# Performance work log

Measured on AMD Instinct MI355X. Metric: run time of the kernel, lower is better.

## Reference

```python
import jax, jax.numpy as jnp
import numpy as np

B, C, T = 64, 22, 2560
U0, U1 = 128, 64  # lstm units per direction


def _lstm(x, Wx, Wh, b, reverse):
    """Keras-style LSTM. x:[B,T,D]. Returns (seq:[B,T,U], last:[B,U])."""
    if reverse:
        x = x[:, ::-1, :]
    U = Wh.shape[0]
    # precompute input projections for all timesteps: [T,B,4U]
    xz = (jnp.einsum('btd,dk->btk', x, Wx) + b).transpose(1, 0, 2)
    h0 = jnp.zeros((x.shape[0], U), x.dtype)
    c0 = jnp.zeros((x.shape[0], U), x.dtype)

    def step(carry, z):
        h, c = carry
        z = z + h @ Wh
        i = jax.nn.sigmoid(z[:, :U])
        f = jax.nn.sigmoid(z[:, U:2 * U])
        g = jnp.tanh(z[:, 2 * U:3 * U])
        o = jax.nn.sigmoid(z[:, 3 * U:])
        c = f * c + i * g
        h = o * jnp.tanh(c)
        return (h, c), h

    (h_last, _), hs = jax.lax.scan(step, (h0, c0), xz)
    hs = hs.transpose(1, 0, 2)  # [B,T,U]
    if reverse:
        hs = hs[:, ::-1, :]
    return hs, h_last


def setup_inputs() -> dict:
    key = jax.random.key(0)
    ks = jax.random.split(key, 20)
    s = 0.05
    d = {"x": jax.random.normal(ks[0], (B, C, T), jnp.float32)}
    # layer 0 (input dim C=22, units U0), fwd + bwd
    d["l0f_Wx"] = jax.random.normal(ks[1], (C, 4 * U0)) * s
    d["l0f_Wh"] = jax.random.normal(ks[2], (U0, 4 * U0)) * s
    d["l0f_b"] = jnp.zeros((4 * U0,))
    d["l0b_Wx"] = jax.random.normal(ks[3], (C, 4 * U0)) * s
    d["l0b_Wh"] = jax.random.normal(ks[4], (U0, 4 * U0)) * s
    d["l0b_b"] = jnp.zeros((4 * U0,))
    # layer 1 (input dim 2*U0=256, units U1), fwd + bwd
    d["l1f_Wx"] = jax.random.normal(ks[5], (2 * U0, 4 * U1)) * s
    d["l1f_Wh"] = jax.random.normal(ks[6], (U1, 4 * U1)) * s
    d["l1f_b"] = jnp.zeros((4 * U1,))
    d["l1b_Wx"] = jax.random.normal(ks[7], (2 * U0, 4 * U1)) * s
    d["l1b_Wh"] = jax.random.normal(ks[8], (U1, 4 * U1)) * s
    d["l1b_b"] = jnp.zeros((4 * U1,))
    # dense head: 2*U1=128 -> 128 -> 64 -> 1
    d["d0_W"] = jax.random.normal(ks[9], (2 * U1, 128)) * s
    d["d0_b"] = jnp.zeros((128,))
    d["d1_W"] = jax.random.normal(ks[10], (128, 64)) * s
    d["d1_b"] = jnp.zeros((64,))
    d["out_W"] = jax.random.normal(ks[11], (64, 1)) * s
    d["out_b"] = jnp.zeros((1,))
    return d


def reference(x, l0f_Wx, l0f_Wh, l0f_b, l0b_Wx, l0b_Wh, l0b_b,
              l1f_Wx, l1f_Wh, l1f_b, l1b_Wx, l1b_Wh, l1b_b,
              d0_W, d0_b, d1_W, d1_b, out_W, out_b):
    h = x.transpose(0, 2, 1)  # [B,T,C]
    # BiLSTM 0, return_sequences=True
    f_seq, _ = _lstm(h, l0f_Wx, l0f_Wh, l0f_b, reverse=False)
    b_seq, _ = _lstm(h, l0b_Wx, l0b_Wh, l0b_b, reverse=True)
    h = jnp.concatenate([f_seq, b_seq], axis=-1)  # [B,T,2*U0]
    # BiLSTM 1, return last state
    _, f_last = _lstm(h, l1f_Wx, l1f_Wh, l1f_b, reverse=False)
    _, b_last = _lstm(h, l1b_Wx, l1b_Wh, l1b_b, reverse=True)
    h = jnp.concatenate([f_last, b_last], axis=-1)  # [B,2*U1]
    # dense head (dropout inactive at inference)
    h = jax.nn.relu(h @ d0_W + d0_b)
    h = jax.nn.relu(h @ d1_W + d1_b)
    return jax.nn.sigmoid(h @ out_W + out_b)  # [B,1]
```

## Files before the change

kernel.cpp:

```cpp
#include <hip/hip_runtime.h>
#include <stdint.h>

#define TT 2560
#define BB 64
#define CC 22

typedef unsigned short ushort_t;
typedef __attribute__((ext_vector_type(4))) float floatx4;
typedef __attribute__((ext_vector_type(8))) short bf16x8;
typedef __attribute__((ext_vector_type(4))) int intx4;

__device__ __forceinline__ float bf2f(ushort_t u){
  union { uint32_t i; float f; } v; v.i = ((uint32_t)u) << 16; return v.f;
}
__device__ __forceinline__ ushort_t f2bf(float f){
  union { float f; uint32_t i; } v; v.f = f;
  uint32_t r = v.i + 0x7FFFu + ((v.i >> 16) & 1u);
  return (ushort_t)(r >> 16);
}
__device__ __forceinline__ float fsig(float x){ return 1.f/(1.f + __expf(-x)); }
__device__ __forceinline__ float ftanh(float x){ return 2.f/(1.f + __expf(-2.f*x)) - 1.f; }

__device__ __forceinline__ void ldsbar(){
  asm volatile("s_waitcnt lgkmcnt(0)\n\ts_barrier" ::: "memory");
}

__global__ __launch_bounds__(256) void k_convert_x(const float* __restrict__ x, ushort_t* __restrict__ xc){
  int i4 = blockIdx.x*256 + threadIdx.x;
  if (i4 >= BB*CC*TT/4) return;
  const float4 v = ((const float4*)x)[i4];
  uint2 o;
  o.x = (uint32_t)f2bf(v.x) | ((uint32_t)f2bf(v.y) << 16);
  o.y = (uint32_t)f2bf(v.z) | ((uint32_t)f2bf(v.w) << 16);
  ((uint2*)xc)[i4] = o;
}

__global__ __launch_bounds__(256) void k_prep_xa(const ushort_t* __restrict__ xc, ushort_t* __restrict__ xA){
  int idx = blockIdx.x*256 + threadIdx.x;
  if (idx >= BB*TT*4) return;
  int q = idx & 3;
  int rest = idx >> 2;
  int t = rest % TT, b = rest / TT;
  ushort_t v[8];
  #pragma unroll
  for (int j=0;j<8;j++){
    int c = q*8 + j;
    v[j] = (c < CC) ? xc[((size_t)b*CC + c)*TT + t] : (ushort_t)0;
  }
  *(uint4*)(xA + (size_t)idx*8) = *(const uint4*)v;
}

__global__ __launch_bounds__(256) void k_wmax(const float* __restrict__ w0f, const float* __restrict__ w0b,
                                              const float* __restrict__ w1f, const float* __restrict__ w1b,
                                              float* __restrict__ scl){
  const int b = blockIdx.x;
  const float* W = (b==0) ? w0f : (b==1) ? w0b : (b==2) ? w1f : w1b;
  const int n = (b < 2) ? 128*512 : 64*256;
  float mx = 0.f;
  for (int i = threadIdx.x; i < n; i += 256) mx = fmaxf(mx, fabsf(W[i]));
  __shared__ float red[256];
  red[threadIdx.x] = mx;
  __syncthreads();
  for (int s = 128; s > 0; s >>= 1){
    if (threadIdx.x < s) red[threadIdx.x] = fmaxf(red[threadIdx.x], red[threadIdx.x+s]);
    __syncthreads();
  }
  if (threadIdx.x == 0) scl[b] = fmaxf(red[0], 1e-8f);
}

__global__ __launch_bounds__(256) void k_prep_l0(const float* __restrict__ WxF, const float* __restrict__ WhF,
                                                 const float* __restrict__ WxB, const float* __restrict__ WhB,
                                                 const float* __restrict__ scl,
                                                 char* __restrict__ W0Q, ushort_t* __restrict__ B0X){
  int idx = blockIdx.x*256 + threadIdx.x;
  if (idx >= 2*512*160) return;
  int dir = idx / 81920; int r0 = idx % 81920; int n = r0 / 160; int k = r0 % 160;
  int g = n >> 7, u = n & 127;
  int wv = u >> 4, qq = (u >> 2) & 3, r = u & 3;
  int row = (qq*8 + wv)*16 + (r*4 + g);
  if (k < 128){
    const float* Wh = dir ? WhB : WhF;
    float sw = scl[dir];
    W0Q[(size_t)dir*65536 + row*128 + k] = (char)(int)rintf(Wh[k*512 + n] * (127.f/sw));
  } else {
    const float* Wx = dir ? WxB : WxF;
    int kx = k - 128;
    float v = (kx < CC) ? Wx[kx*512 + n] : 0.f;
    B0X[(size_t)dir*16384 + row*32 + kx] = f2bf(v);
  }
}

__global__ __launch_bounds__(256) void k_prep_l1(const float* __restrict__ WhF, const float* __restrict__ WhB,
                                                 const float* __restrict__ scl,
                                                 char* __restrict__ W1Q){
  int idx = blockIdx.x*256 + threadIdx.x;
  if (idx >= 2*256*64) return;
  int dir = idx >> 14; int r0 = idx & 16383; int n = r0 >> 6; int k = r0 & 63;
  int g = n >> 6, u = n & 63;
  int wv = u >> 4, qq = (u >> 2) & 3, r = u & 3;
  int row = (qq*4 + wv)*16 + (r*4 + g);
  const float* Wh = dir ? WhB : WhF;
  float sw = scl[2+dir];
  W1Q[(size_t)dir*16384 + row*64 + k] = (char)(int)rintf(Wh[k*256 + n] * (127.f/sw));
}

__global__ __launch_bounds__(256) void k_prep_wxT(const float* __restrict__ Wf, const float* __restrict__ Wb,
                                                  ushort_t* __restrict__ WT){
  int idx = blockIdx.x*256 + threadIdx.x;
  int dir = idx >> 16; int r = idx & 65535; int n = r >> 8; int k = r & 255;
  const float* W = dir ? Wb : Wf;
  WT[idx] = f2bf(W[k*256 + n]);
}

__global__ __launch_bounds__(512, 1) void k_lstm0m(
  const ushort_t* __restrict__ xA, const char* __restrict__ W0Q,
  const ushort_t* __restrict__ B0X, const float* __restrict__ scl,
  const float* __restrict__ bF, const float* __restrict__ bB,
  ushort_t* __restrict__ h0seq)
{
  const int dir = blockIdx.x & 1, b = blockIdx.x >> 1;
  const int tid = threadIdx.x;
  const int wv = tid >> 6, lane = tid & 63, m = lane & 15, q = lane >> 4;
  const int g  = m & 3;
  const int u  = wv*16 + q*4 + (m >> 2);
  const float* bi = dir ? bB : bF;
  const float sclc = scl[dir] * (1.f/16129.f);
  const float em = (g==2) ? -2.f : -1.f;
  const float ym = (g==2) ?  2.f :  1.f;
  const float ya = (g==2) ? -1.f :  0.f;
  const float bzl = bi[g*128 + u];

  __shared__ __align__(16) char AbufC[2][128];

  bf16x8 Bfx[4];
  intx4  BfQ[4][2];
  {
    const ushort_t* Bx = B0X + (size_t)dir*16384;
    const char*     Bq = W0Q + (size_t)dir*65536;
    #pragma unroll
    for (int qt=0; qt<4; qt++){
      int nrow = (qt*8 + wv)*16 + m;
      Bfx[qt] = *(const bf16x8*)(Bx + (size_t)nrow*32 + q*8);
      #pragma unroll
      for (int kt=0; kt<2; kt++)
        BfQ[qt][kt] = *(const intx4*)(Bq + (size_t)nrow*128 + kt*64 + q*16);
    }
  }

  if (tid < 64) ((uint32_t*)AbufC)[tid] = 0u;

  const ushort_t* xap = xA + ((size_t)b*TT*4 + q)*8;
  uint4 px[4];
  #pragma unroll
  for (int j=0; j<4; j++){
    int tj = dir ? (TT-1-j) : j;
    px[j] = *(const uint4*)(xap + (size_t)tj*32);
  }
  const ushort_t* xpp = xap + (size_t)(dir ? (TT-5) : 4)*32;
  const int xstep = dir ? -32 : 32;
  __syncthreads();

  const floatx4 z4 = {0.f,0.f,0.f,0.f};
  const intx4  zi = {0,0,0,0};
  float cst = 0.f;
  const int t00 = dir ? TT-1 : 0;
  ushort_t* hp = h0seq + ((size_t)b*TT + t00)*256 + dir*128 + u;
  const int hstep = dir ? -256 : 256;

  for (int i = 0; i < TT/4; ++i){
    #pragma unroll
    for (int p = 0; p < 4; ++p){
      const int s = i*4 + p;
      const int cur = s & 1, nxt = cur ^ 1;

      const char* ar = &AbufC[cur][0];
      intx4 AfQ0 = *(const intx4*)(ar + q*16);
      intx4 AfQ1 = *(const intx4*)(ar + 64 + q*16);
      bf16x8 Ax = *(const bf16x8*)&px[p];

      floatx4 ax0 = __builtin_amdgcn_mfma_f32_16x16x32_bf16(Ax, Bfx[0], z4, 0,0,0);
      floatx4 ax1 = __builtin_amdgcn_mfma_f32_16x16x32_bf16(Ax, Bfx[1], z4, 0,0,0);
      floatx4 ax2 = __builtin_amdgcn_mfma_f32_16x16x32_bf16(Ax, Bfx[2], z4, 0,0,0);
      floatx4 ax3 = __builtin_amdgcn_mfma_f32_16x16x32_bf16(Ax, Bfx[3], z4, 0,0,0);

      intx4 aq0 = __builtin_amdgcn_mfma_i32_16x16x64_i8(AfQ0, BfQ[0][0], zi, 0,0,0);
      intx4 aq1 = __builtin_amdgcn_mfma_i32_16x16x64_i8(AfQ0, BfQ[1][0], zi, 0,0,0);
      intx4 aq2 = __builtin_amdgcn_mfma_i32_16x16x64_i8(AfQ0, BfQ[2][0], zi, 0,0,0);
      intx4 aq3 = __builtin_amdgcn_mfma_i32_16x16x64_i8(AfQ0, BfQ[3][0], zi, 0,0,0);
      aq0 = __builtin_amdgcn_mfma_i32_16x16x64_i8(AfQ1, BfQ[0][1], aq0, 0,0,0);
      aq1 = __builtin_amdgcn_mfma_i32_16x16x64_i8(AfQ1, BfQ[1][1], aq1, 0,0,0);
      aq2 = __builtin_amdgcn_mfma_i32_16x16x64_i8(AfQ1, BfQ[2][1], aq2, 0,0,0);
      aq3 = __builtin_amdgcn_mfma_i32_16x16x64_i8(AfQ1, BfQ[3][1], aq3, 0,0,0);

      px[p] = *(const uint4*)xpp;
      xpp += xstep;

      float axs = (q < 2) ? ((q == 0) ? ax0[0] : ax1[0])
                          : ((q == 2) ? ax2[0] : ax3[0]);
      int   aqs = (q < 2) ? ((q == 0) ? aq0[0] : aq1[0])
                          : ((q == 2) ? aq2[0] : aq3[0]);

      {
        float z = (float)aqs*sclc + axs + bzl;
        float e = __expf(z * em);
        float y = 1.f/(1.f + e);
        float act = ym*y + ya;

        int ai = __float_as_int(act);
        float sf = __int_as_float(__builtin_amdgcn_ds_swizzle(ai, 0x041F));
        float sg = __int_as_float(__builtin_amdgcn_ds_swizzle(ai, 0x081F));
        float so = __int_as_float(__builtin_amdgcn_ds_swizzle(ai, 0x0C1F));

        float cc = sf*cst + act*sg;
        cst = cc;
        float hl = so*ftanh(cc);
        if (g == 0){
          AbufC[nxt][u] = (char)(int)rintf(hl * 127.f);
          *hp = f2bf(hl);
        }
        hp += hstep;
      }
      ldsbar();
    }
  }
}

__global__ __launch_bounds__(512) void k_xz1_gemm(const ushort_t* __restrict__ h0seq,
                                                  const ushort_t* __restrict__ WxT,
                                                  ushort_t* __restrict__ xz1)
{
  const int mb  = blockIdx.x;
  const int dir = blockIdx.y;
  const ushort_t* W   = WxT + (size_t)dir*256*256;
  ushort_t*       out = xz1 + (size_t)dir*BB*TT*256;
  const int wave = threadIdx.x >> 6;
  const int lane = threadIdx.x & 63;
  const int mw = wave & 3;
  const int nw = wave >> 2;
  const int m_ = lane & 15;
  const int q_ = lane >> 4;

  floatx4 acc[2][8];
  #pragma unroll
  for (int a=0;a<2;a++)
    #pragma unroll
    for (int n=0;n<8;n++) acc[a][n] = (floatx4)0.f;

  const size_t Abase = ((size_t)mb*128 + mw*32 + m_)*256 + q_*8;
  const size_t Bbase = ((size_t)nw*128 + m_)*256 + q_*8;

  for (int kc = 0; kc < 256; kc += 32){
    bf16x8 afr[2];
    #pragma unroll
    for (int mt=0;mt<2;mt++)
      afr[mt] = *(const bf16x8*)(h0seq + Abase + (size_t)mt*16*256 + kc);
    #pragma unroll
    for (int nt=0;nt<8;nt++){
      bf16x8 bfr = *(const bf16x8*)(W + Bbase + (size_t)nt*16*256 + kc);
      #pragma unroll
      for (int mt=0;mt<2;mt++)
        acc[mt][nt] = __builtin_amdgcn_mfma_f32_16x16x32_bf16(afr[mt], bfr, acc[mt][nt], 0,0,0);
    }
  }
  #pragma unroll
  for (int mt=0;mt<2;mt++)
    #pragma unroll
    for (int r=0;r<4;r++){
      size_t bt = (size_t)mb*128 + mw*32 + mt*16 + q_*4 + r;
      ushort_t* rowp = out + bt*256;
      #pragma unroll
      for (int wvz=0; wvz<4; wvz++){
        uint32_t lo = f2bf(acc[mt][wvz][r]);
        uint32_t hi = f2bf(acc[mt][wvz+4][r]);
        *(uint32_t*)(rowp + (wvz*16+m_)*4 + 2*nw) = lo | (hi << 16);
      }
    }
}

__global__ __launch_bounds__(256, 1) void k_lstm1m(
  const ushort_t* __restrict__ xz1R,
  const char* __restrict__ W1Q,
  const float* __restrict__ scl,
  const float* __restrict__ bF, const float* __restrict__ bB,
  float* __restrict__ h1last)
{
  const int dir = blockIdx.x & 1, b = blockIdx.x >> 1;
  const int tid = threadIdx.x;
  const int wv = tid >> 6, lane = tid & 63, m = lane & 15, q = lane >> 4;
  const int g = m & 3;
  const int u = wv*16 + q*4 + (m >> 2);
  const float* bi = dir ? bB : bF;
  const float sclc = scl[2+dir] * (1.f/16129.f);
  const float em = (g==2) ? -2.f : -1.f;
  const float ym = (g==2) ?  2.f :  1.f;
  const float ya = (g==2) ? -1.f :  0.f;
  const float bzl = bi[g*64 + u];

  __shared__ __align__(16) char HbufC[2][64];

  intx4 BfQ[4];
  {
    const char* Bq = W1Q + (size_t)dir*16384;
    #pragma unroll
    for (int qt=0; qt<4; qt++)
      BfQ[qt] = *(const intx4*)(Bq + (size_t)((qt*4 + wv)*16 + m)*64 + q*16);
  }

  if (tid < 32) ((uint32_t*)HbufC)[tid] = 0u;

  const ushort_t* xzr = xz1R + ((size_t)dir*BB + b)*TT*256 + (size_t)(u*4 + g);
  ushort_t pz[4];
  #pragma unroll
  for (int j=0; j<4; j++){
    int tj = dir ? (TT-1-j) : j;
    pz[j] = xzr[(size_t)tj*256];
  }
  const ushort_t* xpp = xzr + (size_t)(dir ? (TT-5) : 4)*256;
  const int zstep = dir ? -256 : 256;
  __syncthreads();

  const intx4 zi = {0,0,0,0};
  float cst = 0.f, hl = 0.f;

  for (int i = 0; i < TT/4; ++i){
    #pragma unroll
    for (int p = 0; p < 4; ++p){
      const int s = i*4 + p;
      const int cur = s & 1, nxt = cur ^ 1;

      intx4 AfQ = *(const intx4*)(&HbufC[cur][0] + q*16);

      float w = bzl + bf2f(pz[p]);
      pz[p] = *xpp;
      xpp += zstep;

      intx4 c0 = __builtin_amdgcn_mfma_i32_16x16x64_i8(AfQ, BfQ[0], zi, 0,0,0);
      intx4 c1 = __builtin_amdgcn_mfma_i32_16x16x64_i8(AfQ, BfQ[1], zi, 0,0,0);
      intx4 c2 = __builtin_amdgcn_mfma_i32_16x16x64_i8(AfQ, BfQ[2], zi, 0,0,0);
      intx4 c3 = __builtin_amdgcn_mfma_i32_16x16x64_i8(AfQ, BfQ[3], zi, 0,0,0);

      int aqs = (q < 2) ? ((q == 0) ? c0[0] : c1[0])
                        : ((q == 2) ? c2[0] : c3[0]);

      {
        float z = (float)aqs*sclc + w;
        float e = __expf(z * em);
        float y = 1.f/(1.f + e);
        float act = ym*y + ya;

        int ai = __float_as_int(act);
        float sf = __int_as_float(__builtin_amdgcn_ds_swizzle(ai, 0x041F));
        float sg = __int_as_float(__builtin_amdgcn_ds_swizzle(ai, 0x081F));
        float so = __int_as_float(__builtin_amdgcn_ds_swizzle(ai, 0x0C1F));

        float cc = sf*cst + act*sg;
        cst = cc;
        hl = so*ftanh(cc);
        if (g == 0) HbufC[nxt][u] = (char)(int)rintf(hl * 127.f);
      }
      ldsbar();
    }
  }
  if (g == 0) h1last[(size_t)b*128 + dir*64 + u] = hl;
}

__global__ __launch_bounds__(128) void k_head(
  const float* __restrict__ h1last,
  const float* __restrict__ d0W, const float* __restrict__ d0b,
  const float* __restrict__ d1W, const float* __restrict__ d1b,
  const float* __restrict__ oW,  const float* __restrict__ ob,
  float* __restrict__ outp)
{
  const int b = blockIdx.x;
  const int j = threadIdx.x;
  __shared__ float v0[128], v1[128];
  v0[j] = h1last[b*128 + j];
  __syncthreads();
  float acc = d0b[j];
  #pragma unroll
  for (int k=0;k<128;k++) acc += v0[k]*d0W[k*128 + j];
  v1[j] = fmaxf(acc, 0.f);
  __syncthreads();
  if (j < 64){
    float a2 = d1b[j];
    #pragma unroll
    for (int k=0;k<128;k++) a2 += v1[k]*d1W[k*64 + j];
    float p = fmaxf(a2, 0.f) * oW[j];
    #pragma unroll
    for (int off=32; off>0; off>>=1) p += __shfl_down(p, off, 64);
    if (j == 0) outp[b] = 1.f/(1.f + __expf(-(p + ob[0])));
  }
}

extern "C" void kernel_launch(void* const* d_in, const int* in_sizes, int n_in,
                              void* d_out, int out_size, void* d_ws, size_t ws_size,
                              hipStream_t stream)
{
  const float* x     = (const float*)d_in[0];
  const float* l0fWx = (const float*)d_in[1];
  const float* l0fWh = (const float*)d_in[2];
  const float* l0fb  = (const float*)d_in[3];
  const float* l0bWx = (const float*)d_in[4];
  const float* l0bWh = (const float*)d_in[5];
  const float* l0bb  = (const float*)d_in[6];
  const float* l1fWx = (const float*)d_in[7];
  const float* l1fWh = (const float*)d_in[8];
  const float* l1fb  = (const float*)d_in[9];
  const float* l1bWx = (const float*)d_in[10];
  const float* l1bWh = (const float*)d_in[11];
  const float* l1bb  = (const float*)d_in[12];
  const float* d0W = (const float*)d_in[13];
  const float* d0b = (const float*)d_in[14];
  const float* d1W = (const float*)d_in[15];
  const float* d1b = (const float*)d_in[16];
  const float* oW  = (const float*)d_in[17];
  const float* ob  = (const float*)d_in[18];
  float* outp = (float*)d_out;

  char* ws = (char*)d_ws;
  const size_t OFF_XT  = 0;
  const size_t OFF_SCL = 7208960ull;
  const size_t OFF_H0  = OFF_XT  + 7864320ull;
  const size_t OFF_XZ  = OFF_H0  + 83886080ull;
  const size_t OFF_XA  = OFF_XZ;
  const size_t OFF_WT  = OFF_XZ  + 167772160ull;
  const size_t OFF_B0  = OFF_WT  + 262144ull;
  const size_t OFF_B0X = OFF_B0  + 131072ull;
  const size_t OFF_B1  = OFF_B0  + 327680ull;
  const size_t OFF_H1  = OFF_B1  + 65536ull;

  ushort_t* xc  = (ushort_t*)(ws + OFF_XT);
  float*    sclp= (float*)(ws + OFF_SCL);
  ushort_t* h0  = (ushort_t*)(ws + OFF_H0);
  ushort_t* xz1 = (ushort_t*)(ws + OFF_XZ);
  ushort_t* xA  = (ushort_t*)(ws + OFF_XA);
  ushort_t* WT  = (ushort_t*)(ws + OFF_WT);
  char*     W0Q = (char*)(ws + OFF_B0);
  ushort_t* B0X = (ushort_t*)(ws + OFF_B0X);
  char*     W1Q = (char*)(ws + OFF_B1);
  float*    h1l = (float*)(ws + OFF_H1);

  hipLaunchKernelGGL(k_convert_x,   dim3(3520), dim3(256), 0, stream, x, xc);
  hipLaunchKernelGGL(k_prep_xa,     dim3(2560), dim3(256), 0, stream, xc, xA);
  hipLaunchKernelGGL(k_wmax,        dim3(4),    dim3(256), 0, stream, l0fWh, l0bWh, l1fWh, l1bWh, sclp);
  hipLaunchKernelGGL(k_prep_l0,     dim3(640),  dim3(256), 0, stream, l0fWx, l0fWh, l0bWx, l0bWh, sclp, W0Q, B0X);
  hipLaunchKernelGGL(k_prep_l1,     dim3(128),  dim3(256), 0, stream, l1fWh, l1bWh, sclp, W1Q);
  hipLaunchKernelGGL(k_prep_wxT,    dim3(512),  dim3(256), 0, stream, l1fWx, l1bWx, WT);
  hipLaunchKernelGGL(k_lstm0m,      dim3(128),  dim3(512), 0, stream, xA, W0Q, B0X, sclp, l0fb, l0bb, h0);
  hipLaunchKernelGGL(k_xz1_gemm,    dim3(1280,2), dim3(512), 0, stream, h0, WT, xz1);
  hipLaunchKernelGGL(k_lstm1m,      dim3(128),  dim3(256), 0, stream, xz1, W1Q, sclp, l1fb, l1bb, h1l);
  hipLaunchKernelGGL(k_head,        dim3(64),   dim3(128), 0, stream,
                     h1l, d0W, d0b, d1W, d1b, oW, ob, outp);
}
```

Baseline: 2.106 ms.

## Replace per-step MFMA recurrences with per-lane int8 dot4 and fp32 input FMAs

In both LSTM recurrent kernels, the int8 MFMA instructions for the h@Wh product are replaced by a per-lane sdot4 loop over the full hidden vector read from LDS. Each lane now owns one gate row, so weights are stored row-contiguous instead of in the MFMA-swizzled layout. Layer 0's input projection becomes 22 fp32 FMAs per lane against an fp32 x buffer instead of a bf16 MFMA. The aim is to remove MFMA issue and result latency from the serial per-timestep dependency chain. In exchange there are many more VALU ops per step, wider register use and a larger fp32 x buffer.

```diff
diff --git a/kernel.cpp b/kernel.cpp
--- a/kernel.cpp
+++ b/kernel.cpp
@@ -23,6 +23,20 @@
 
 __device__ __forceinline__ void ldsbar(){
   asm volatile("s_waitcnt lgkmcnt(0)\n\ts_barrier" ::: "memory");
+}
+
+__device__ __forceinline__ int dot4(int a, int b, int acc){
+#if __has_builtin(__builtin_amdgcn_sdot4)
+  return __builtin_amdgcn_sdot4(a, b, acc, false);
+#else
+  #pragma unroll
+  for (int j=0;j<4;j++){
+    int av = (int)(char)(a >> (8*j));
+    int bv = (int)(char)(b >> (8*j));
+    acc += av*bv;
+  }
+  return acc;
+#endif
 }
 
 __global__ __launch_bounds__(256) void k_convert_x(const float* __restrict__ x, ushort_t* __restrict__ xc){
@@ -35,19 +49,15 @@
   ((uint2*)xc)[i4] = o;
 }
 
-__global__ __launch_bounds__(256) void k_prep_xa(const ushort_t* __restrict__ xc, ushort_t* __restrict__ xA){
+__global__ __launch_bounds__(256) void k_prep_xa(const ushort_t* __restrict__ xc, float* __restrict__ xAf){
   int idx = blockIdx.x*256 + threadIdx.x;
-  if (idx >= BB*TT*4) return;
-  int q = idx & 3;
-  int rest = idx >> 2;
+  if (idx >= BB*TT*24) return;
+  int c = idx % 24;
+  int rest = idx / 24;
   int t = rest % TT, b = rest / TT;
-  ushort_t v[8];
-  #pragma unroll
-  for (int j=0;j<8;j++){
-    int c = q*8 + j;
-    v[j] = (c < CC) ? xc[((size_t)b*CC + c)*TT + t] : (ushort_t)0;
-  }
-  *(uint4*)(xA + (size_t)idx*8) = *(const uint4*)v;
+  float v = 0.f;
+  if (c < CC) v = bf2f(xc[((size_t)b*CC + c)*TT + t]);
+  xAf[idx] = v;
 }
 
 __global__ __launch_bounds__(256) void k_wmax(const float* __restrict__ w0f, const float* __restrict__ w0b,
@@ -71,22 +81,20 @@
 __global__ __launch_bounds__(256) void k_prep_l0(const float* __restrict__ WxF, const float* __restrict__ WhF,
                                                  const float* __restrict__ WxB, const float* __restrict__ WhB,
                                                  const float* __restrict__ scl,
-                                                 char* __restrict__ W0Q, ushort_t* __restrict__ B0X){
+                                                 char* __restrict__ W0Qd, float* __restrict__ W0Xf){
   int idx = blockIdx.x*256 + threadIdx.x;
   if (idx >= 2*512*160) return;
   int dir = idx / 81920; int r0 = idx % 81920; int n = r0 / 160; int k = r0 % 160;
-  int g = n >> 7, u = n & 127;
-  int wv = u >> 4, qq = (u >> 2) & 3, r = u & 3;
-  int row = (qq*8 + wv)*16 + (r*4 + g);
   if (k < 128){
     const float* Wh = dir ? WhB : WhF;
     float sw = scl[dir];
-    W0Q[(size_t)dir*65536 + row*128 + k] = (char)(int)rintf(Wh[k*512 + n] * (127.f/sw));
+    W0Qd[(size_t)dir*65536 + n*128 + k] = (char)(int)rintf(Wh[k*512 + n] * (127.f/sw));
   } else {
-    const float* Wx = dir ? WxB : WxF;
     int kx = k - 128;
-    float v = (kx < CC) ? Wx[kx*512 + n] : 0.f;
-    B0X[(size_t)dir*16384 + row*32 + kx] = f2bf(v);
+    if (kx < 24){
+      const float* Wx = dir ? WxB : WxF;
+      W0Xf[(size_t)dir*12288 + n*24 + kx] = (kx < CC) ? Wx[kx*512 + n] : 0.f;
+    }
   }
 }
 
@@ -95,13 +103,10 @@
                                                  char* __restrict__ W1Q){
   int idx = blockIdx.x*256 + threadIdx.x;
   if (idx >= 2*256*64) return;
-  int dir = idx >> 14; int r0 = idx & 16383; int n = r0 >> 6; int k = r0 & 63;
-  int g = n >> 6, u = n & 63;
-  int wv = u >> 4, qq = (u >> 2) & 3, r = u & 3;
-  int row = (qq*4 + wv)*16 + (r*4 + g);
+  int dir = idx >> 14; int r = idx & 16383; int n = r >> 6; int k = r & 63;
   const float* Wh = dir ? WhB : WhF;
   float sw = scl[2+dir];
-  W1Q[(size_t)dir*16384 + row*64 + k] = (char)(int)rintf(Wh[k*256 + n] * (127.f/sw));
+  W1Q[(size_t)dir*16384 + n*64 + k] = (char)(int)rintf(Wh[k*256 + n] * (127.f/sw));
 }
 
 __global__ __launch_bounds__(256) void k_prep_wxT(const float* __restrict__ Wf, const float* __restrict__ Wb,
@@ -113,8 +118,8 @@
 }
 
 __global__ __launch_bounds__(512, 1) void k_lstm0m(
-  const ushort_t* __restrict__ xA, const char* __restrict__ W0Q,
-  const ushort_t* __restrict__ B0X, const float* __restrict__ scl,
+  const float* __restrict__ xAf, const char* __restrict__ W0Qd,
+  const float* __restrict__ W0Xf, const float* __restrict__ scl,
   const float* __restrict__ bF, const float* __restrict__ bB,
   ushort_t* __restrict__ h0seq)
 {
@@ -123,45 +128,46 @@
   const int wv = tid >> 6, lane = tid & 63, m = lane & 15, q = lane >> 4;
   const int g  = m & 3;
   const int u  = wv*16 + q*4 + (m >> 2);
+  const int n  = g*128 + u;
   const float* bi = dir ? bB : bF;
   const float sclc = scl[dir] * (1.f/16129.f);
   const float em = (g==2) ? -2.f : -1.f;
   const float ym = (g==2) ?  2.f :  1.f;
   const float ya = (g==2) ? -1.f :  0.f;
-  const float bzl = bi[g*128 + u];
+  const float bzl = bi[n];
 
   __shared__ __align__(16) char AbufC[2][128];
 
-  bf16x8 Bfx[4];
-  intx4  BfQ[4][2];
+  intx4 Wd[8];
   {
-    const ushort_t* Bx = B0X + (size_t)dir*16384;
-    const char*     Bq = W0Q + (size_t)dir*65536;
-    #pragma unroll
-    for (int qt=0; qt<4; qt++){
-      int nrow = (qt*8 + wv)*16 + m;
-      Bfx[qt] = *(const bf16x8*)(Bx + (size_t)nrow*32 + q*8);
-      #pragma unroll
-      for (int kt=0; kt<2; kt++)
-        BfQ[qt][kt] = *(const intx4*)(Bq + (size_t)nrow*128 + kt*64 + q*16);
-    }
+    const char* Wq = W0Qd + (size_t)dir*65536 + (size_t)n*128;
+    #pragma unroll
+    for (int c=0; c<8; c++) Wd[c] = ((const intx4*)Wq)[c];
+  }
+  float Wxr[22];
+  {
+    const float* wxp = W0Xf + (size_t)dir*12288 + (size_t)n*24;
+    #pragma unroll
+    for (int c=0; c<22; c++) Wxr[c] = wxp[c];
   }
 
   if (tid < 64) ((uint32_t*)AbufC)[tid] = 0u;
 
-  const ushort_t* xap = xA + ((size_t)b*TT*4 + q)*8;
-  uint4 px[4];
-  #pragma unroll
-  for (int j=0; j<4; j++){
-    int tj = dir ? (TT-1-j) : j;
-    px[j] = *(const uint4*)(xap + (size_t)tj*32);
-  }
-  const ushort_t* xpp = xap + (size_t)(dir ? (TT-5) : 4)*32;
-  const int xstep = dir ? -32 : 32;
+  const float* xap = xAf + (size_t)b*TT*24;
+  float4 xv0[6], xv1[6];
+  {
+    int t0 = dir ? (TT-1) : 0;
+    int t1 = dir ? (TT-2) : 1;
+    #pragma unroll
+    for (int c=0; c<6; c++){
+      xv0[c] = ((const float4*)(xap + (size_t)t0*24))[c];
+      xv1[c] = ((const float4*)(xap + (size_t)t1*24))[c];
+    }
+  }
+  const float* xpp = xap + (size_t)(dir ? (TT-3) : 2)*24;
+  const int xstep = dir ? -24 : 24;
   __syncthreads();
 
-  const floatx4 z4 = {0.f,0.f,0.f,0.f};
-  const intx4  zi = {0,0,0,0};
   float cst = 0.f;
   const int t00 = dir ? TT-1 : 0;
   ushort_t* hp = h0seq + ((size_t)b*TT + t00)*256 + dir*128 + u;
@@ -173,35 +179,38 @@
       const int s = i*4 + p;
       const int cur = s & 1, nxt = cur ^ 1;
 
-      const char* ar = &AbufC[cur][0];
-      intx4 AfQ0 = *(const intx4*)(ar + q*16);
-      intx4 AfQ1 = *(const intx4*)(ar + 64 + q*16);
-      bf16x8 Ax = *(const bf16x8*)&px[p];
-
-      floatx4 ax0 = __builtin_amdgcn_mfma_f32_16x16x32_bf16(Ax, Bfx[0], z4, 0,0,0);
-      floatx4 ax1 = __builtin_amdgcn_mfma_f32_16x16x32_bf16(Ax, Bfx[1], z4, 0,0,0);
-      floatx4 ax2 = __builtin_amdgcn_mfma_f32_16x16x32_bf16(Ax, Bfx[2], z4, 0,0,0);
-      floatx4 ax3 = __builtin_amdgcn_mfma_f32_16x16x32_bf16(Ax, Bfx[3], z4, 0,0,0);
-
-      intx4 aq0 = __builtin_amdgcn_mfma_i32_16x16x64_i8(AfQ0, BfQ[0][0], zi, 0,0,0);
-      intx4 aq1 = __builtin_amdgcn_mfma_i32_16x16x64_i8(AfQ0, BfQ[1][0], zi, 0,0,0);
-      intx4 aq2 = __builtin_amdgcn_mfma_i32_16x16x64_i8(AfQ0, BfQ[2][0], zi, 0,0,0);
-      intx4 aq3 = __builtin_amdgcn_mfma_i32_16x16x64_i8(AfQ0, BfQ[3][0], zi, 0,0,0);
-      aq0 = __builtin_amdgcn_mfma_i32_16x16x64_i8(AfQ1, BfQ[0][1], aq0, 0,0,0);
-      aq1 = __builtin_amdgcn_mfma_i32_16x16x64_i8(AfQ1, BfQ[1][1], aq1, 0,0,0);
-      aq2 = __builtin_amdgcn_mfma_i32_16x16x64_i8(AfQ1, BfQ[2][1], aq2, 0,0,0);
-      aq3 = __builtin_amdgcn_mfma_i32_16x16x64_i8(AfQ1, BfQ[3][1], aq3, 0,0,0);
-
-      px[p] = *(const uint4*)xpp;
-      xpp += xstep;
-
-      float axs = (q < 2) ? ((q == 0) ? ax0[0] : ax1[0])
-                          : ((q == 2) ? ax2[0] : ax3[0]);
-      int   aqs = (q < 2) ? ((q == 0) ? aq0[0] : aq1[0])
-                          : ((q == 2) ? aq2[0] : aq3[0]);
-
-      {
-        float z = (float)aqs*sclc + axs + bzl;
+      intx4 H[8];
+      {
+        const intx4* hv = (const intx4*)&AbufC[cur][0];
+        #pragma unroll
+        for (int c=0; c<8; c++) H[c] = hv[c];
+      }
+
+      float zx = bzl;
+      {
+        const float* xf = (p & 1) ? (const float*)xv1 : (const float*)xv0;
+        #pragma unroll
+        for (int c=0; c<22; c++) zx = fmaf(xf[c], Wxr[c], zx);
+      }
+      {
+        float4* xs = (p & 1) ? xv1 : xv0;
+        #pragma unroll
+        for (int c=0; c<6; c++) xs[c] = ((const float4*)xpp)[c];
+        xpp += xstep;
+      }
+
+      int e0 = 0, e1 = 0, e2 = 0, e3 = 0;
+      #pragma unroll
+      for (int c=0; c<8; c++){
+        e0 = dot4(H[c][0], Wd[c][0], e0);
+        e1 = dot4(H[c][1], Wd[c][1], e1);
+        e2 = dot4(H[c][2], Wd[c][2], e2);
+        e3 = dot4(H[c][3], Wd[c][3], e3);
+      }
+      int acc = (e0 + e1) + (e2 + e3);
+
+      {
+        float z = (float)acc*sclc + zx;
         float e = __expf(z * em);
         float y = 1.f/(1.f + e);
         float act = ym*y + ya;
@@ -289,21 +298,21 @@
   const int wv = tid >> 6, lane = tid & 63, m = lane & 15, q = lane >> 4;
   const int g = m & 3;
   const int u = wv*16 + q*4 + (m >> 2);
+  const int n = g*64 + u;
   const float* bi = dir ? bB : bF;
   const float sclc = scl[2+dir] * (1.f/16129.f);
   const float em = (g==2) ? -2.f : -1.f;
   const float ym = (g==2) ?  2.f :  1.f;
   const float ya = (g==2) ? -1.f :  0.f;
-  const float bzl = bi[g*64 + u];
+  const float bzl = bi[n];
 
   __shared__ __align__(16) char HbufC[2][64];
 
-  intx4 BfQ[4];
+  intx4 Wd[4];
   {
-    const char* Bq = W1Q + (size_t)dir*16384;
-    #pragma unroll
-    for (int qt=0; qt<4; qt++)
-      BfQ[qt] = *(const intx4*)(Bq + (size_t)((qt*4 + wv)*16 + m)*64 + q*16);
+    const char* Wq = W1Q + (size_t)dir*16384 + (size_t)n*64;
+    #pragma unroll
+    for (int c=0; c<4; c++) Wd[c] = ((const intx4*)Wq)[c];
   }
 
   if (tid < 32) ((uint32_t*)HbufC)[tid] = 0u;
@@ -319,7 +328,6 @@
   const int zstep = dir ? -256 : 256;
   __syncthreads();
 
-  const intx4 zi = {0,0,0,0};
   float cst = 0.f, hl = 0.f;
 
   for (int i = 0; i < TT/4; ++i){
@@ -328,22 +336,29 @@
       const int s = i*4 + p;
       const int cur = s & 1, nxt = cur ^ 1;
 
-      intx4 AfQ = *(const intx4*)(&HbufC[cur][0] + q*16);
+      intx4 H[4];
+      {
+        const intx4* hv = (const intx4*)&HbufC[cur][0];
+        #pragma unroll
+        for (int c=0; c<4; c++) H[c] = hv[c];
+      }
 
       float w = bzl + bf2f(pz[p]);
       pz[p] = *xpp;
       xpp += zstep;
 
-      intx4 c0 = __builtin_amdgcn_mfma_i32_16x16x64_i8(AfQ, BfQ[0], zi, 0,0,0);
-      intx4 c1 = __builtin_amdgcn_mfma_i32_16x16x64_i8(AfQ, BfQ[1], zi, 0,0,0);
-      intx4 c2 = __builtin_amdgcn_mfma_i32_16x16x64_i8(AfQ, BfQ[2], zi, 0,0,0);
-      intx4 c3 = __builtin_amdgcn_mfma_i32_16x16x64_i8(AfQ, BfQ[3], zi, 0,0,0);
-
-      int aqs = (q < 2) ? ((q == 0) ? c0[0] : c1[0])
-                        : ((q == 2) ? c2[0] : c3[0]);
-
-      {
-        float z = (float)aqs*sclc + w;
+      int e0 = 0, e1 = 0, e2 = 0, e3 = 0;
+      #pragma unroll
+      for (int c=0; c<4; c++){
+        e0 = dot4(H[c][0], Wd[c][0], e0);
+        e1 = dot4(H[c][1], Wd[c][1], e1);
+        e2 = dot4(H[c][2], Wd[c][2], e2);
+        e3 = dot4(H[c][3], Wd[c][3], e3);
+      }
+      int acc = (e0 + e1) + (e2 + e3);
+
+      {
+        float z = (float)acc*sclc + w;
         float e = __expf(z * em);
         float y = 1.f/(1.f + e);
         float act = ym*y + ya;
@@ -433,20 +448,20 @@
   float*    sclp= (float*)(ws + OFF_SCL);
   ushort_t* h0  = (ushort_t*)(ws + OFF_H0);
   ushort_t* xz1 = (ushort_t*)(ws + OFF_XZ);
-  ushort_t* xA  = (ushort_t*)(ws + OFF_XA);
+  float*    xAf = (float*)(ws + OFF_XA);
   ushort_t* WT  = (ushort_t*)(ws + OFF_WT);
-  char*     W0Q = (char*)(ws + OFF_B0);
-  ushort_t* B0X = (ushort_t*)(ws + OFF_B0X);
+  char*     W0Qd= (char*)(ws + OFF_B0);
+  float*    W0Xf= (float*)(ws + OFF_B0X);
   char*     W1Q = (char*)(ws + OFF_B1);
   float*    h1l = (float*)(ws + OFF_H1);
 
   hipLaunchKernelGGL(k_convert_x,   dim3(3520), dim3(256), 0, stream, x, xc);
-  hipLaunchKernelGGL(k_prep_xa,     dim3(2560), dim3(256), 0, stream, xc, xA);
+  hipLaunchKernelGGL(k_prep_xa,     dim3(15360), dim3(256), 0, stream, xc, xAf);
   hipLaunchKernelGGL(k_wmax,        dim3(4),    dim3(256), 0, stream, l0fWh, l0bWh, l1fWh, l1bWh, sclp);
-  hipLaunchKernelGGL(k_prep_l0,     dim3(640),  dim3(256), 0, stream, l0fWx, l0fWh, l0bWx, l0bWh, sclp, W0Q, B0X);
+  hipLaunchKernelGGL(k_prep_l0,     dim3(640),  dim3(256), 0, stream, l0fWx, l0fWh, l0bWx, l0bWh, sclp, W0Qd, W0Xf);
   hipLaunchKernelGGL(k_prep_l1,     dim3(128),  dim3(256), 0, stream, l1fWh, l1bWh, sclp, W1Q);
   hipLaunchKernelGGL(k_prep_wxT,    dim3(512),  dim3(256), 0, stream, l1fWx, l1bWx, WT);
-  hipLaunchKernelGGL(k_lstm0m,      dim3(128),  dim3(512), 0, stream, xA, W0Q, B0X, sclp, l0fb, l0bb, h0);
+  hipLaunchKernelGGL(k_lstm0m,      dim3(128),  dim3(512), 0, stream, xAf, W0Qd, W0Xf, sclp, l0fb, l0bb, h0);
   hipLaunchKernelGGL(k_xz1_gemm,    dim3(1280,2), dim3(512), 0, stream, h0, WT, xz1);
   hipLaunchKernelGGL(k_lstm1m,      dim3(128),  dim3(256), 0, stream, xz1, W1Q, sclp, l1fb, l1bb, h1l);
   hipLaunchKernelGGL(k_head,        dim3(64),   dim3(128), 0, stream,
```

After: 2.946 ms. 1.4x slower.
